# Performance work log

Hardware: AMD Instinct MI355X
Metric: run time of the kernel (lower is better)

The kernel has to match this reference:

```python
import jax, jax.numpy as jnp
import numpy as np

B, S, DIM = 2, 2048, 2048
N_HEADS, N_KV_HEADS = 16, 4
HEAD_DIM = DIM // N_HEADS  # 128
N_REP = N_HEADS // N_KV_HEADS  # 4
ROPE_THETA = 10000.0


def setup_inputs() -> dict:
    key = jax.random.key(0)
    ks = jax.random.split(key, 6)
    x = jax.random.normal(ks[0], (B, S, DIM), dtype=jnp.float32)
    # torch nn.Linear weights are [out_features, in_features]
    sc = 0.02
    wq = jax.random.normal(ks[1], (N_HEADS * HEAD_DIM, DIM), dtype=jnp.float32) * sc
    wk = jax.random.normal(ks[2], (N_KV_HEADS * HEAD_DIM, DIM), dtype=jnp.float32) * sc
    wv = jax.random.normal(ks[3], (N_KV_HEADS * HEAD_DIM, DIM), dtype=jnp.float32) * sc
    wo = jax.random.normal(ks[4], (DIM, N_HEADS * HEAD_DIM), dtype=jnp.float32) * sc
    # precomputed rotary table (freqs_cis in llama): [S, head_dim//2]
    inv_freq = 1.0 / (ROPE_THETA ** (jnp.arange(0, HEAD_DIM, 2, dtype=jnp.float32) / HEAD_DIM))
    t = jnp.arange(S, dtype=jnp.float32)
    freqs = jnp.outer(t, inv_freq)  # [S, head_dim//2]
    freqs_cos = jnp.cos(freqs)
    freqs_sin = jnp.sin(freqs)
    # additive causal mask as passed to SDPA (float, 0 on allowed, -inf-like elsewhere)
    causal = jnp.tril(jnp.ones((S, S), dtype=bool))
    mask = jnp.where(causal, 0.0, -1e9).astype(jnp.float32)
    return {"x": x, "wq": wq, "wk": wk, "wv": wv, "wo": wo,
            "freqs_cos": freqs_cos, "freqs_sin": freqs_sin, "mask": mask}


def _apply_rope(t, cos, sin):
    # t: [B, S, H, D]; cos/sin: [S, D//2] -> complex multiply on adjacent pairs
    tr = t.reshape(*t.shape[:-1], -1, 2)  # [B,S,H,D/2,2]
    tre, tim = tr[..., 0], tr[..., 1]
    c = cos[None, :, None, :]
    s = sin[None, :, None, :]
    out_re = tre * c - tim * s
    out_im = tre * s + tim * c
    return jnp.stack([out_re, out_im], axis=-1).reshape(t.shape)


def reference(x, wq, wk, wv, wo, freqs_cos, freqs_sin, mask):
    Bx, Sx, _ = x.shape
    xq = (x @ wq.T).reshape(Bx, Sx, N_HEADS, HEAD_DIM)
    xk = (x @ wk.T).reshape(Bx, Sx, N_KV_HEADS, HEAD_DIM)
    xv = (x @ wv.T).reshape(Bx, Sx, N_KV_HEADS, HEAD_DIM)
    xq = _apply_rope(xq, freqs_cos, freqs_sin)
    xk = _apply_rope(xk, freqs_cos, freqs_sin)
    # repeat_kv for GQA: [B,S,KV,D] -> [B,S,KV*n_rep,D]
    keys = jnp.repeat(xk, N_REP, axis=2)
    values = jnp.repeat(xv, N_REP, axis=2)
    q = xq.transpose(0, 2, 1, 3)      # [B,H,S,D]
    k = keys.transpose(0, 2, 1, 3)
    v = values.transpose(0, 2, 1, 3)
    scale = 1.0 / jnp.sqrt(jnp.float32(HEAD_DIM))
    scores = jnp.einsum('bhqd,bhkd->bhqk', q, k) * scale + mask[None, None]
    attn = jax.nn.softmax(scores, axis=-1)
    out = jnp.einsum('bhqk,bhkd->bhqd', attn, v)
    out = out.transpose(0, 2, 1, 3).reshape(Bx, Sx, -1)
    return out @ wo.T
```

## Files before the change

kernel.cpp:

```cpp
#include <hip/hip_runtime.h>
#include <hip/hip_bf16.h>

#define B_   2
#define S_   2048
#define DIM_ 2048
#define NH   16
#define NKV  4
#define HD   128
#define QKVN 3072

typedef __attribute__((ext_vector_type(8)))  short  sv8;
typedef __attribute__((ext_vector_type(8)))  ushort usv8;
typedef __attribute__((ext_vector_type(4)))  float  fv4;
typedef __attribute__((ext_vector_type(16))) float  fv16;

__device__ __forceinline__ float fast_exp2(float x) {
  return __builtin_amdgcn_exp2f(x);
}

__device__ __forceinline__ ushort f2bf(float f) {
  __hip_bfloat16 h = __float2bfloat16(f);
  union { __hip_bfloat16 h; ushort u; } c; c.h = h; return c.u;
}
__device__ __forceinline__ float bf2f(ushort u) {
  union { unsigned int i; float f; } c; c.i = ((unsigned)u) << 16; return c.f;
}

__device__ __forceinline__ unsigned int cvtpk(float lo, float hi) {
  unsigned int r;
  asm("v_cvt_pk_bf16_f32 %0, %1, %2" : "=v"(r) : "v"(lo), "v"(hi));
  return r;
}
__device__ __forceinline__ unsigned int xhalf(unsigned int x) {
  return (unsigned int)__shfl_xor((int)x, 32, 64);
}

__device__ __forceinline__ float tmax16(const fv16& v) {
  float a = fmaxf(fmaxf(v[0], v[1]),  fmaxf(v[2], v[3]));
  float b = fmaxf(fmaxf(v[4], v[5]),  fmaxf(v[6], v[7]));
  float c = fmaxf(fmaxf(v[8], v[9]),  fmaxf(v[10], v[11]));
  float d = fmaxf(fmaxf(v[12], v[13]), fmaxf(v[14], v[15]));
  return fmaxf(fmaxf(a, b), fmaxf(c, d));
}
__device__ __forceinline__ float tsum16(const fv16& v) {
  float a = (v[0] + v[1]) + (v[2] + v[3]);
  float b = (v[4] + v[5]) + (v[6] + v[7]);
  float c = (v[8] + v[9]) + (v[10] + v[11]);
  float d = (v[12] + v[13]) + (v[14] + v[15]);
  return (a + b) + (c + d);
}

__device__ __forceinline__ void async16(const void* g, void* l) {
  __builtin_amdgcn_global_load_lds(
      (const __attribute__((address_space(1))) unsigned int*)g,
      (__attribute__((address_space(3))) unsigned int*)l, 16, 0, 0);
}

__global__ void cvt_kernel(const float* __restrict__ in, ushort* __restrict__ out, int n) {
  int i = (blockIdx.x * 256 + threadIdx.x) * 4;
  if (i >= n) return;
  fv4 v = *(const fv4*)(in + i);
  ushort4 o;
  o.x = f2bf(v[0]); o.y = f2bf(v[1]); o.z = f2bf(v[2]); o.w = f2bf(v[3]);
  *(ushort4*)(out + i) = o;
}

__global__ void rope_kernel(const ushort* __restrict__ raw, const float* __restrict__ fc,
                            const float* __restrict__ fs, ushort* __restrict__ out,
                            int heads, int rowstride, float scale) {
  int t = blockIdx.x * 256 + threadIdx.x;
  int grp = t & 15;
  int h   = (t >> 4) % heads;
  int s   = ((t >> 4) / heads) % S_;
  int b   = t / (16 * heads * S_);
  const ushort* src = raw + (size_t)(b * S_ + s) * rowstride + h * HD + grp * 8;
  sv8 v = *(const sv8*)src;
  fv4 c  = *(const fv4*)(fc + s * 64 + grp * 4);
  fv4 sn = *(const fv4*)(fs + s * 64 + grp * 4);
  sv8 o;
#pragma unroll
  for (int p = 0; p < 4; ++p) {
    float re = bf2f((ushort)v[2 * p]);
    float im = bf2f((ushort)v[2 * p + 1]);
    float orr = (re * c[p] - im * sn[p]) * scale;
    float oi  = (re * sn[p] + im * c[p]) * scale;
    o[2 * p]     = (short)f2bf(orr);
    o[2 * p + 1] = (short)f2bf(oi);
  }
  ushort* dst = out + ((size_t)(b * heads + h) * S_ + s) * HD + grp * 8;
  *(sv8*)dst = o;
}

__global__ __launch_bounds__(256) void vtrans_kernel(const ushort* __restrict__ vraw,
                                                     ushort* __restrict__ vt, int rowstride) {
  __shared__ ushort tile[128][136];
  int blk = blockIdx.x;
  int st  = blk & 15;
  int kvb = blk >> 4;
  int kv  = kvb & 3;
  int b   = kvb >> 2;
  int s0  = st << 7;
#pragma unroll
  for (int it = 0; it < 8; ++it) {
    int t = it * 256 + threadIdx.x;
    int srow = t >> 4;
    int d8 = (t & 15) * 8;
    usv8 v = *(const usv8*)(vraw + (size_t)(b * S_ + s0 + srow) * rowstride + kv * HD + d8);
#pragma unroll
    for (int j = 0; j < 8; ++j) tile[d8 + j][srow] = v[j];
  }
  __syncthreads();
#pragma unroll
  for (int it = 0; it < 8; ++it) {
    int t = it * 256 + threadIdx.x;
    int d = t >> 4;
    int s8 = (t & 15) * 8;
    usv8 o;
#pragma unroll
    for (int j = 0; j < 8; ++j) o[j] = tile[d][s8 + j];
    *(usv8*)(vt + ((size_t)(b * NKV + kv) * HD + d) * S_ + s0 + s8) = o;
  }
}

template <typename OutT>
__global__ __launch_bounds__(512, 2) void gemm256(const ushort* __restrict__ A,
                                                  const ushort* __restrict__ Bm,
                                                  OutT* __restrict__ C,
                                                  int M, int N, int K) {
  __shared__ __align__(16) ushort SM[65536];
  int nb = N >> 8;
  int bx = blockIdx.x % nb, by = blockIdx.x / nb;
  int m0 = by << 8, n0 = bx << 8;
  int tid = threadIdx.x;
  int lane = tid & 63, w = tid >> 6;
  int l15 = lane & 15, lg = lane >> 4;
  int wm = (w >> 2) * 128;
  int wn = (w & 3) * 64;
  int pA = (w >> 2);
  int pB = 2 + ((w & 3) >> 1);
  int brow0 = (w & 1) * 64;

  int srow = tid >> 3;
  int cb   = ((tid & 7) * 16) ^ ((srow & 7) << 4);
  const ushort* sA0 = A  + (size_t)(m0 + srow) * K + (cb >> 1);
  const ushort* sB0 = Bm + (size_t)(n0 + srow) * K + (cb >> 1);
  const ushort* srcs[4] = { sA0, sA0 + (size_t)128 * K, sB0, sB0 + (size_t)128 * K };
  size_t rstep = (size_t)64 * K;

  int nkt = K >> 6;

  auto STG = [&](int part, int t, int db) {
    ushort* d0 = SM + db * 32768 + part * 8192 + (w << 9);
    const ushort* s0 = srcs[part] + t * 64;
    async16(s0, d0);
    async16(s0 + rstep, d0 + 4096);
  };

  fv4 acc[8][4] = {};
  sv8 a[4][2], b[2][2], b2[2][2];

#pragma unroll
  for (int p = 0; p < 4; ++p) STG(p, 0, 0);
  {
    int t1 = 1 < nkt ? 1 : 0;
#pragma unroll
    for (int p = 0; p < 4; ++p) STG(p, t1, 1);
  }
  asm volatile("s_waitcnt vmcnt(8)");
  __builtin_amdgcn_s_barrier();

  for (int t = 0; t < nkt; ++t) {
    int db = t & 1;
    int t2 = t + 2 < nkt ? t + 2 : nkt - 1;
    const char* Ab = (const char*)SM + db * 65536 + pA * 16384;
    const char* Bb = (const char*)SM + db * 65536 + pB * 16384;

#pragma unroll
    for (int m = 0; m < 4; ++m)
#pragma unroll
      for (int kk = 0; kk < 2; ++kk) {
        int row = m * 16 + l15;
        a[m][kk] = *(const sv8*)(Ab + row * 128 + ((kk * 64 + lg * 16) ^ ((row & 7) << 4)));
      }
#pragma unroll
    for (int j = 0; j < 2; ++j)
#pragma unroll
      for (int kk = 0; kk < 2; ++kk) {
        int row = brow0 + j * 16 + l15;
        b[j][kk] = *(const sv8*)(Bb + row * 128 + ((kk * 64 + lg * 16) ^ ((row & 7) << 4)));
      }
    __builtin_amdgcn_s_barrier();
    asm volatile("s_waitcnt lgkmcnt(0)");
    __builtin_amdgcn_s_setprio(1);
#pragma unroll
    for (int m = 0; m < 4; ++m)
#pragma unroll
      for (int j = 0; j < 2; ++j)
#pragma unroll
        for (int kk = 0; kk < 2; ++kk)
          acc[m][j] = __builtin_amdgcn_mfma_f32_16x16x32_bf16(a[m][kk], b[j][kk], acc[m][j], 0, 0, 0);
    __builtin_amdgcn_s_setprio(0);
    __builtin_amdgcn_s_barrier();

#pragma unroll
    for (int j = 0; j < 2; ++j)
#pragma unroll
      for (int kk = 0; kk < 2; ++kk) {
        int row = brow0 + (j + 2) * 16 + l15;
        b2[j][kk] = *(const sv8*)(Bb + row * 128 + ((kk * 64 + lg * 16) ^ ((row & 7) << 4)));
      }
    __builtin_amdgcn_s_barrier();
    asm volatile("s_waitcnt lgkmcnt(0)");
    __builtin_amdgcn_s_setprio(1);
#pragma unroll
    for (int m = 0; m < 4; ++m)
#pragma unroll
      for (int j = 0; j < 2; ++j)
#pragma unroll
        for (int kk = 0; kk < 2; ++kk)
          acc[m][j + 2] = __builtin_amdgcn_mfma_f32_16x16x32_bf16(a[m][kk], b2[j][kk], acc[m][j + 2], 0, 0, 0);
    __builtin_amdgcn_s_setprio(0);
    __builtin_amdgcn_s_barrier();

#pragma unroll
    for (int m = 0; m < 4; ++m)
#pragma unroll
      for (int kk = 0; kk < 2; ++kk) {
        int row = 64 + m * 16 + l15;
        a[m][kk] = *(const sv8*)(Ab + row * 128 + ((kk * 64 + lg * 16) ^ ((row & 7) << 4)));
      }
    STG(2, t2, db);
    STG(3, t2, db);
    __builtin_amdgcn_s_barrier();
    asm volatile("s_waitcnt lgkmcnt(0)");
    __builtin_amdgcn_s_setprio(1);
#pragma unroll
    for (int m = 0; m < 4; ++m)
#pragma unroll
      for (int j = 0; j < 2; ++j)
#pragma unroll
        for (int kk = 0; kk < 2; ++kk)
          acc[m + 4][j + 2] = __builtin_amdgcn_mfma_f32_16x16x32_bf16(a[m][kk], b2[j][kk], acc[m + 4][j + 2], 0, 0, 0);
    __builtin_amdgcn_s_setprio(0);
    __builtin_amdgcn_s_barrier();

    STG(0, t2, db);
    STG(1, t2, db);
    asm volatile("s_waitcnt vmcnt(8)");
    __builtin_amdgcn_s_barrier();
    __builtin_amdgcn_s_setprio(1);
#pragma unroll
    for (int m = 0; m < 4; ++m)
#pragma unroll
      for (int j = 0; j < 2; ++j)
#pragma unroll
        for (int kk = 0; kk < 2; ++kk)
          acc[m + 4][j] = __builtin_amdgcn_mfma_f32_16x16x32_bf16(a[m][kk], b[j][kk], acc[m + 4][j], 0, 0, 0);
    __builtin_amdgcn_s_setprio(0);
    __builtin_amdgcn_s_barrier();
  }

  asm volatile("s_waitcnt vmcnt(0)");
#pragma unroll
  for (int m = 0; m < 8; ++m)
#pragma unroll
    for (int j = 0; j < 4; ++j)
#pragma unroll
      for (int r = 0; r < 4; ++r) {
        int row = m0 + wm + m * 16 + lg * 4 + r;
        int col = n0 + wn + j * 16 + l15;
        if constexpr (sizeof(OutT) == 2) C[(size_t)row * N + col] = (OutT)f2bf(acc[m][j][r]);
        else                             C[(size_t)row * N + col] = (OutT)acc[m][j][r];
      }
}

__global__ __launch_bounds__(512, 2) void attn_kernel(const ushort* __restrict__ Q,
                                                      const ushort* __restrict__ Kr,
                                                      const ushort* __restrict__ Vt,
                                                      ushort* __restrict__ O) {
  __shared__ __align__(16) ushort SMEM[65536];

  int blk = blockIdx.x;
  int bh  = blk & 31;
  int pr  = blk >> 5;
  int h   = bh & 15;
  int b   = bh >> 4;
  int kv  = h >> 2;
  int lane = threadIdx.x & 63, w = threadIdx.x >> 6;
  int wg = w & 3, Hf = w >> 2;
  int l31 = lane & 31, hh = lane >> 5;

  const ushort* Qbase = Q  + (size_t)(b * NH  + h ) * S_ * HD;
  const ushort* Kbase = Kr + (size_t)(b * NKV + kv) * S_ * HD;
  const ushort* Vbase = Vt + (size_t)(b * NKV + kv) * HD * S_;

  const ushort* kSrc[4]; ushort* kDst[2][4];
  const ushort* vSrc[4]; ushort* vDst[2][4];
#pragma unroll
  for (int it = 0; it < 4; ++it) {
    int lin = it * 4096 + wg * 1024 + lane * 16;
    { int row = lin >> 8; int cbv = (lin & 255) ^ ((row & 7) << 4);
      kSrc[it] = Kbase + (size_t)row * HD + (cbv >> 1); }
    { int row = lin >> 7; int cbv = (lin & 127) ^ ((row & 7) << 4);
      vSrc[it] = Vbase + (size_t)row * S_ + (cbv >> 1); }
#pragma unroll
    for (int buf = 0; buf < 2; ++buf) {
      kDst[buf][it] = SMEM + Hf * 16384 + buf * 8192 + ((it * 4096 + wg * 1024) >> 1);
      vDst[buf][it] = SMEM + 32768 + Hf * 16384 + buf * 8192 + ((it * 4096 + wg * 1024) >> 1);
    }
  }

  float* cML = (float*)SMEM;
  float* cO  = (float*)SMEM + 512;

  for (int pass = 0; pass < 2; ++pass) {
    int qt = pass ? (15 - pr) : pr;
    int q0 = qt << 7;
    int qrow_w = q0 + wg * 32;
    int myq    = qrow_w + l31;
    int nj     = qt + 1;
    int ktbase = Hf * nj;

    sv8 qf[8];
#pragma unroll
    for (int kk = 0; kk < 8; ++kk)
      qf[kk] = *(const sv8*)(Qbase + (size_t)myq * HD + kk * 16 + hh * 8);

    fv16 oacc[4] = {};
    float mrun = -1e30f, lrun = 0.f;

    {
      size_t k0 = (size_t)ktbase << 6;
#pragma unroll
      for (int it = 0; it < 4; ++it) async16(kSrc[it] + k0 * HD, kDst[0][it]);
#pragma unroll
      for (int it = 0; it < 4; ++it) async16(vSrc[it] + k0,      vDst[0][it]);
    }

    for (int j = 0; j < nj; ++j) {
      int cur = j & 1, nxt = cur ^ 1;
      __syncthreads();
      if (j + 1 < nj) {
        size_t k0n = (size_t)(ktbase + j + 1) << 6;
#pragma unroll
        for (int it = 0; it < 4; ++it) async16(kSrc[it] + k0n * HD, kDst[nxt][it]);
#pragma unroll
        for (int it = 0; it < 4; ++it) async16(vSrc[it] + k0n,      vDst[nxt][it]);
      }
      const char* KsC = (const char*)(SMEM + Hf * 16384 + cur * 8192);
      const char* VsC = (const char*)(SMEM + 32768 + Hf * 16384 + cur * 8192);
      int k0 = (ktbase + j) << 6;

      fv16 sacc[2] = {};
      __builtin_amdgcn_s_setprio(1);
#pragma unroll
      for (int kk = 0; kk < 8; ++kk) {
        int cbq = kk * 32 + hh * 16;
        int r0 = l31, r1 = 32 + l31;
        sv8 kf0 = *(const sv8*)(KsC + r0 * 256 + (cbq ^ ((r0 & 7) << 4)));
        sv8 kf1 = *(const sv8*)(KsC + r1 * 256 + (cbq ^ ((r1 & 7) << 4)));
        sacc[0] = __builtin_amdgcn_mfma_f32_32x32x16_bf16(kf0, qf[kk], sacc[0], 0, 0, 0);
        sacc[1] = __builtin_amdgcn_mfma_f32_32x32x16_bf16(kf1, qf[kk], sacc[1], 0, 0, 0);
      }
      __builtin_amdgcn_s_setprio(0);

      if (k0 + 63 > qrow_w) {
        int thr = myq - k0 - 4 * hh;
#pragma unroll
        for (int t = 0; t < 2; ++t)
#pragma unroll
          for (int r = 0; r < 16; ++r) {
            int kp = t * 32 + (r & 3) + 8 * (r >> 2);
            if (kp > thr) sacc[t][r] = -1e38f;
          }
      }

      float tmax = fmaxf(tmax16(sacc[0]), tmax16(sacc[1]));
      tmax = fmaxf(tmax, __shfl_xor(tmax, 32, 64));

      if (__any(tmax > mrun + 8.0f)) {
        float mnew = fmaxf(mrun, tmax);
        float esc  = fast_exp2(mrun - mnew);
        lrun *= esc;
        float er[16];
#pragma unroll
        for (int r = 0; r < 16; ++r) er[r] = __shfl(esc, (r & 3) + 8 * (r >> 2) + 4 * hh, 64);
#pragma unroll
        for (int d0 = 0; d0 < 4; ++d0)
#pragma unroll
          for (int r = 0; r < 16; ++r) oacc[d0][r] *= er[r];
        mrun = mnew;
      }

#pragma unroll
      for (int t = 0; t < 2; ++t)
#pragma unroll
        for (int r = 0; r < 16; ++r) sacc[t][r] = fast_exp2(sacc[t][r] - mrun);
      float psum = tsum16(sacc[0]) + tsum16(sacc[1]);
      psum += __shfl_xor(psum, 32, 64);
      lrun += psum;

      union Frag { unsigned int u[4]; sv8 v; } pa[4];
#pragma unroll
      for (int t = 0; t < 2; ++t)
#pragma unroll
        for (int half = 0; half < 2; ++half) {
          int cbq = half * 8;
          unsigned int a0 = cvtpk(sacc[t][cbq + 0], sacc[t][cbq + 1]);
          unsigned int a1 = cvtpk(sacc[t][cbq + 2], sacc[t][cbq + 3]);
          unsigned int b0 = cvtpk(sacc[t][cbq + 4], sacc[t][cbq + 5]);
          unsigned int b1 = cvtpk(sacc[t][cbq + 6], sacc[t][cbq + 7]);
          unsigned int a0p = xhalf(a0), a1p = xhalf(a1);
          unsigned int b0p = xhalf(b0), b1p = xhalf(b1);
          pa[2 * t + half].u[0] = hh ? b0p : a0;
          pa[2 * t + half].u[1] = hh ? b1p : a1;
          pa[2 * t + half].u[2] = hh ? b0  : a0p;
          pa[2 * t + half].u[3] = hh ? b1  : a1p;
        }

      __builtin_amdgcn_s_setprio(1);
#pragma unroll
      for (int ks = 0; ks < 4; ++ks) {
        int cbq = ks * 32 + hh * 16;
#pragma unroll
        for (int d0 = 0; d0 < 4; ++d0) {
          int row = d0 * 32 + l31;
          sv8 vf = *(const sv8*)(VsC + row * 128 + (cbq ^ ((row & 7) << 4)));
          oacc[d0] = __builtin_amdgcn_mfma_f32_32x32x16_bf16(pa[ks].v, vf, oacc[d0], 0, 0, 0);
        }
      }
      __builtin_amdgcn_s_setprio(0);
    }

    __syncthreads();
    if (Hf) {
      int base = wg * 64 + lane;
      cML[base * 2]     = mrun;
      cML[base * 2 + 1] = lrun;
      float* dst = cO + base * 65;
#pragma unroll
      for (int d0 = 0; d0 < 4; ++d0)
#pragma unroll
        for (int r = 0; r < 16; ++r) dst[d0 * 16 + r] = oacc[d0][r];
    }
    __syncthreads();
    if (!Hf) {
      int base = wg * 64 + lane;
      float m2 = cML[base * 2], l2 = cML[base * 2 + 1];
      const float* src = cO + base * 65;
      float m  = fmaxf(mrun, m2);
      float e1 = fast_exp2(mrun - m), e2 = fast_exp2(m2 - m);
      float l  = lrun * e1 + l2 * e2;
      float inv = 1.0f / l;
      float f1 = e1 * inv, f2 = e2 * inv;
      float f1b[16], f2b[16];
#pragma unroll
      for (int r = 0; r < 16; ++r) {
        int ro = (r & 3) + 8 * (r >> 2) + 4 * hh;
        f1b[r] = __shfl(f1, ro, 64);
        f2b[r] = __shfl(f2, ro, 64);
      }
#pragma unroll
      for (int r = 0; r < 16; ++r) {
        int q = qrow_w + (r & 3) + 8 * (r >> 2) + 4 * hh;
#pragma unroll
        for (int d0 = 0; d0 < 4; ++d0) {
          int d = d0 * 32 + l31;
          float val = oacc[d0][r] * f1b[r] + src[d0 * 16 + r] * f2b[r];
          O[(size_t)(b * S_ + q) * DIM_ + h * HD + d] = f2bf(val);
        }
      }
    }
    __syncthreads();
  }
}

extern "C" void kernel_launch(void* const* d_in, const int* in_sizes, int n_in,
                              void* d_out, int out_size, void* d_ws, size_t ws_size,
                              hipStream_t stream) {
  const float* x  = (const float*)d_in[0];
  const float* wq = (const float*)d_in[1];
  const float* wk = (const float*)d_in[2];
  const float* wv = (const float*)d_in[3];
  const float* wo = (const float*)d_in[4];
  const float* fc = (const float*)d_in[5];
  const float* fs = (const float*)d_in[6];
  float* out = (float*)d_out;

  char* ws = (char*)d_ws;
  size_t off = 0;
  auto alloc = [&](size_t bytes) -> ushort* {
    ushort* p = (ushort*)(ws + off);
    off += (bytes + 255) & ~(size_t)255;
    return p;
  };
  ushort* xb    = alloc((size_t)B_ * S_ * DIM_ * 2);
  ushort* wqkvb = alloc((size_t)QKVN * DIM_ * 2);
  ushort* wob   = alloc((size_t)DIM_ * DIM_ * 2);
  ushort* qkvr  = alloc((size_t)B_ * S_ * QKVN * 2);
  ushort* qr    = alloc((size_t)B_ * S_ * DIM_ * 2);
  ushort* kr    = alloc((size_t)B_ * S_ * NKV * HD * 2);
  ushort* vtb   = alloc((size_t)B_ * S_ * NKV * HD * 2);
  ushort* obf   = alloc((size_t)B_ * S_ * DIM_ * 2);
  (void)ws_size; (void)n_in; (void)in_sizes; (void)out_size;

  cvt_kernel<<<(B_ * S_ * DIM_) / 1024, 256, 0, stream>>>(x,  xb, B_ * S_ * DIM_);
  cvt_kernel<<<(DIM_ * DIM_) / 1024,     256, 0, stream>>>(wq, wqkvb,                 DIM_ * DIM_);
  cvt_kernel<<<(NKV * HD * DIM_) / 1024, 256, 0, stream>>>(wk, wqkvb + 2048 * DIM_,   NKV * HD * DIM_);
  cvt_kernel<<<(NKV * HD * DIM_) / 1024, 256, 0, stream>>>(wv, wqkvb + 2560 * DIM_,   NKV * HD * DIM_);
  cvt_kernel<<<(DIM_ * DIM_) / 1024,     256, 0, stream>>>(wo, wob, DIM_ * DIM_);

  gemm256<ushort><<<(B_ * S_ / 256) * (QKVN / 256), 512, 0, stream>>>(xb, wqkvb, qkvr,
                                                                     B_ * S_, QKVN, DIM_);

  const float qscale = 0.08838834764831845f * 1.4426950408889634f;
  rope_kernel<<<(B_ * S_ * NH  * 16) / 256, 256, 0, stream>>>(qkvr,        fc, fs, qr, NH,  QKVN, qscale);
  rope_kernel<<<(B_ * S_ * NKV * 16) / 256, 256, 0, stream>>>(qkvr + 2048, fc, fs, kr, NKV, QKVN, 1.0f);
  vtrans_kernel<<<B_ * NKV * (S_ / 128), 256, 0, stream>>>(qkvr + 2560, vtb, QKVN);

  attn_kernel<<<B_ * NH * 8, 512, 0, stream>>>(qr, kr, vtb, obf);

  gemm256<float><<<(B_ * S_ / 256) * (DIM_ / 256), 512, 0, stream>>>(obf, wob, out, B_ * S_, DIM_, DIM_);
}
```

Baseline: 210.5 us.

## Use smaller GEMM tiles so QKV and output projections fill all CUs

New measurement: 196.4 us. 6.7% less time.

```diff
diff --git a/kernel.cpp b/kernel.cpp
--- a/kernel.cpp
+++ b/kernel.cpp
@@ -123,57 +123,128 @@
 }
 
 template <typename OutT>
-__global__ __launch_bounds__(512, 2) void gemm256(const ushort* __restrict__ A,
-                                                  const ushort* __restrict__ Bm,
-                                                  OutT* __restrict__ C,
-                                                  int M, int N, int K) {
-  __shared__ __align__(16) ushort SM[65536];
-  int nb = N >> 8;
+__global__ __launch_bounds__(256) void gemm_bt(const ushort* __restrict__ A,
+                                               const ushort* __restrict__ Bm,
+                                               OutT* __restrict__ C,
+                                               int M, int N, int K) {
+  __shared__ ushort As[128 * 64];
+  __shared__ ushort Bs[128 * 64];
+  int nb = N >> 7;
+  int bx = blockIdx.x % nb;
+  int by = blockIdx.x / nb;
+  int m0 = by << 7, n0 = bx << 7;
+  int lane = threadIdx.x & 63, w = threadIdx.x >> 6;
+  int l15 = lane & 15, lg = lane >> 4;
+  int wm = (w >> 1) * 64, wn = (w & 1) * 64;
+
+  const ushort* aSrc[4]; const ushort* bSrc[4];
+  ushort* aDst[4]; ushort* bDst[4];
+#pragma unroll
+  for (int it = 0; it < 4; ++it) {
+    int lin = it * 4096 + w * 1024 + lane * 16;
+    int row = lin >> 7;
+    int cb  = (lin & 127) ^ ((row & 7) << 4);
+    aSrc[it] = A  + (size_t)(m0 + row) * K + (cb >> 1);
+    bSrc[it] = Bm + (size_t)(n0 + row) * K + (cb >> 1);
+    aDst[it] = As + ((it * 4096 + w * 1024) >> 1);
+    bDst[it] = Bs + ((it * 4096 + w * 1024) >> 1);
+  }
+
+  fv4 acc[4][4] = {};
+
+  for (int kt = 0; kt < K; kt += 64) {
+#pragma unroll
+    for (int it = 0; it < 4; ++it) async16(aSrc[it] + kt, aDst[it]);
+#pragma unroll
+    for (int it = 0; it < 4; ++it) async16(bSrc[it] + kt, bDst[it]);
+    __syncthreads();
+#pragma unroll
+    for (int kk = 0; kk < 2; ++kk) {
+      sv8 af[4], bfr[4];
+#pragma unroll
+      for (int i = 0; i < 4; ++i) {
+        int row = wm + i * 16 + l15;
+        int byt = row * 128 + ((kk * 64 + (lg << 4)) ^ ((row & 7) << 4));
+        af[i] = *(const sv8*)((const char*)As + byt);
+      }
+#pragma unroll
+      for (int j = 0; j < 4; ++j) {
+        int row = wn + j * 16 + l15;
+        int byt = row * 128 + ((kk * 64 + (lg << 4)) ^ ((row & 7) << 4));
+        bfr[j] = *(const sv8*)((const char*)Bs + byt);
+      }
+#pragma unroll
+      for (int i = 0; i < 4; ++i)
+#pragma unroll
+        for (int j = 0; j < 4; ++j)
+          acc[i][j] = __builtin_amdgcn_mfma_f32_16x16x32_bf16(af[i], bfr[j], acc[i][j], 0, 0, 0);
+    }
+    __syncthreads();
+  }
+
+#pragma unroll
+  for (int i = 0; i < 4; ++i)
+#pragma unroll
+    for (int j = 0; j < 4; ++j)
+#pragma unroll
+      for (int r = 0; r < 4; ++r) {
+        int row = m0 + wm + i * 16 + (lg << 2) + r;
+        int col = n0 + wn + j * 16 + l15;
+        if constexpr (sizeof(OutT) == 2) C[(size_t)row * N + col] = (OutT)f2bf(acc[i][j][r]);
+        else                             C[(size_t)row * N + col] = (OutT)acc[i][j][r];
+      }
+}
+
+template <typename OutT>
+__global__ __launch_bounds__(512) void gemmOP(const ushort* __restrict__ A,
+                                              const ushort* __restrict__ Bm,
+                                              OutT* __restrict__ C,
+                                              int M, int N, int K) {
+  __shared__ __align__(16) ushort SM[49152];
+  int nb = N >> 7;
   int bx = blockIdx.x % nb, by = blockIdx.x / nb;
-  int m0 = by << 8, n0 = bx << 8;
+  int m0 = by << 8, n0 = bx << 7;
   int tid = threadIdx.x;
   int lane = tid & 63, w = tid >> 6;
   int l15 = lane & 15, lg = lane >> 4;
   int wm = (w >> 2) * 128;
-  int wn = (w & 3) * 64;
+  int wn = (w & 3) * 32;
   int pA = (w >> 2);
-  int pB = 2 + ((w & 3) >> 1);
-  int brow0 = (w & 1) * 64;
 
   int srow = tid >> 3;
   int cb   = ((tid & 7) * 16) ^ ((srow & 7) << 4);
   const ushort* sA0 = A  + (size_t)(m0 + srow) * K + (cb >> 1);
   const ushort* sB0 = Bm + (size_t)(n0 + srow) * K + (cb >> 1);
-  const ushort* srcs[4] = { sA0, sA0 + (size_t)128 * K, sB0, sB0 + (size_t)128 * K };
+  const ushort* srcs[3] = { sA0, sA0 + (size_t)128 * K, sB0 };
   size_t rstep = (size_t)64 * K;
 
   int nkt = K >> 6;
 
   auto STG = [&](int part, int t, int db) {
-    ushort* d0 = SM + db * 32768 + part * 8192 + (w << 9);
+    ushort* d0 = SM + db * 24576 + part * 8192 + (w << 9);
     const ushort* s0 = srcs[part] + t * 64;
     async16(s0, d0);
     async16(s0 + rstep, d0 + 4096);
   };
 
-  fv4 acc[8][4] = {};
-  sv8 a[4][2], b[2][2], b2[2][2];
-
-#pragma unroll
-  for (int p = 0; p < 4; ++p) STG(p, 0, 0);
+  fv4 acc[8][2] = {};
+  sv8 a[4][2], b[2], b2[2];
+
+#pragma unroll
+  for (int p = 0; p < 3; ++p) STG(p, 0, 0);
   {
     int t1 = 1 < nkt ? 1 : 0;
 #pragma unroll
-    for (int p = 0; p < 4; ++p) STG(p, t1, 1);
-  }
-  asm volatile("s_waitcnt vmcnt(8)");
+    for (int p = 0; p < 3; ++p) STG(p, t1, 1);
+  }
+  asm volatile("s_waitcnt vmcnt(6)");
   __builtin_amdgcn_s_barrier();
 
   for (int t = 0; t < nkt; ++t) {
     int db = t & 1;
     int t2 = t + 2 < nkt ? t + 2 : nkt - 1;
-    const char* Ab = (const char*)SM + db * 65536 + pA * 16384;
-    const char* Bb = (const char*)SM + db * 65536 + pB * 16384;
+    const char* Ab = (const char*)SM + db * 49152 + pA * 16384;
+    const char* Bb = (const char*)SM + db * 49152 + 32768;
 
 #pragma unroll
     for (int m = 0; m < 4; ++m)
@@ -183,42 +254,34 @@
         a[m][kk] = *(const sv8*)(Ab + row * 128 + ((kk * 64 + lg * 16) ^ ((row & 7) << 4)));
       }
 #pragma unroll
-    for (int j = 0; j < 2; ++j)
-#pragma unroll
-      for (int kk = 0; kk < 2; ++kk) {
-        int row = brow0 + j * 16 + l15;
-        b[j][kk] = *(const sv8*)(Bb + row * 128 + ((kk * 64 + lg * 16) ^ ((row & 7) << 4)));
-      }
+    for (int kk = 0; kk < 2; ++kk) {
+      int row = wn + l15;
+      b[kk] = *(const sv8*)(Bb + row * 128 + ((kk * 64 + lg * 16) ^ ((row & 7) << 4)));
+    }
     __builtin_amdgcn_s_barrier();
     asm volatile("s_waitcnt lgkmcnt(0)");
     __builtin_amdgcn_s_setprio(1);
 #pragma unroll
     for (int m = 0; m < 4; ++m)
 #pragma unroll
-      for (int j = 0; j < 2; ++j)
-#pragma unroll
-        for (int kk = 0; kk < 2; ++kk)
-          acc[m][j] = __builtin_amdgcn_mfma_f32_16x16x32_bf16(a[m][kk], b[j][kk], acc[m][j], 0, 0, 0);
+      for (int kk = 0; kk < 2; ++kk)
+        acc[m][0] = __builtin_amdgcn_mfma_f32_16x16x32_bf16(a[m][kk], b[kk], acc[m][0], 0, 0, 0);
     __builtin_amdgcn_s_setprio(0);
     __builtin_amdgcn_s_barrier();
 
 #pragma unroll
-    for (int j = 0; j < 2; ++j)
-#pragma unroll
-      for (int kk = 0; kk < 2; ++kk) {
-        int row = brow0 + (j + 2) * 16 + l15;
-        b2[j][kk] = *(const sv8*)(Bb + row * 128 + ((kk * 64 + lg * 16) ^ ((row & 7) << 4)));
-      }
+    for (int kk = 0; kk < 2; ++kk) {
+      int row = wn + 16 + l15;
+      b2[kk] = *(const sv8*)(Bb + row * 128 + ((kk * 64 + lg * 16) ^ ((row & 7) << 4)));
+    }
     __builtin_amdgcn_s_barrier();
     asm volatile("s_waitcnt lgkmcnt(0)");
     __builtin_amdgcn_s_setprio(1);
 #pragma unroll
     for (int m = 0; m < 4; ++m)
 #pragma unroll
-      for (int j = 0; j < 2; ++j)
-#pragma unroll
-        for (int kk = 0; kk < 2; ++kk)
-          acc[m][j + 2] = __builtin_amdgcn_mfma_f32_16x16x32_bf16(a[m][kk], b2[j][kk], acc[m][j + 2], 0, 0, 0);
+      for (int kk = 0; kk < 2; ++kk)
+        acc[m][1] = __builtin_amdgcn_mfma_f32_16x16x32_bf16(a[m][kk], b2[kk], acc[m][1], 0, 0, 0);
     __builtin_amdgcn_s_setprio(0);
     __builtin_amdgcn_s_barrier();
 
@@ -230,32 +293,27 @@
         a[m][kk] = *(const sv8*)(Ab + row * 128 + ((kk * 64 + lg * 16) ^ ((row & 7) << 4)));
       }
     STG(2, t2, db);
-    STG(3, t2, db);
     __builtin_amdgcn_s_barrier();
     asm volatile("s_waitcnt lgkmcnt(0)");
     __builtin_amdgcn_s_setprio(1);
 #pragma unroll
     for (int m = 0; m < 4; ++m)
 #pragma unroll
-      for (int j = 0; j < 2; ++j)
-#pragma unroll
-        for (int kk = 0; kk < 2; ++kk)
-          acc[m + 4][j + 2] = __builtin_amdgcn_mfma_f32_16x16x32_bf16(a[m][kk], b2[j][kk], acc[m + 4][j + 2], 0, 0, 0);
+      for (int kk = 0; kk < 2; ++kk)
+        acc[m + 4][1] = __builtin_amdgcn_mfma_f32_16x16x32_bf16(a[m][kk], b2[kk], acc[m + 4][1], 0, 0, 0);
     __builtin_amdgcn_s_setprio(0);
     __builtin_amdgcn_s_barrier();
 
     STG(0, t2, db);
     STG(1, t2, db);
-    asm volatile("s_waitcnt vmcnt(8)");
+    asm volatile("s_waitcnt vmcnt(6)");
     __builtin_amdgcn_s_barrier();
     __builtin_amdgcn_s_setprio(1);
 #pragma unroll
     for (int m = 0; m < 4; ++m)
 #pragma unroll
-      for (int j = 0; j < 2; ++j)
-#pragma unroll
-        for (int kk = 0; kk < 2; ++kk)
-          acc[m + 4][j] = __builtin_amdgcn_mfma_f32_16x16x32_bf16(a[m][kk], b[j][kk], acc[m + 4][j], 0, 0, 0);
+      for (int kk = 0; kk < 2; ++kk)
+        acc[m + 4][0] = __builtin_amdgcn_mfma_f32_16x16x32_bf16(a[m][kk], b[kk], acc[m + 4][0], 0, 0, 0);
     __builtin_amdgcn_s_setprio(0);
     __builtin_amdgcn_s_barrier();
   }
@@ -264,7 +322,7 @@
 #pragma unroll
   for (int m = 0; m < 8; ++m)
 #pragma unroll
-    for (int j = 0; j < 4; ++j)
+    for (int j = 0; j < 2; ++j)
 #pragma unroll
       for (int r = 0; r < 4; ++r) {
         int row = m0 + wm + m * 16 + lg * 4 + r;
@@ -510,7 +568,7 @@
   cvt_kernel<<<(NKV * HD * DIM_) / 1024, 256, 0, stream>>>(wv, wqkvb + 2560 * DIM_,   NKV * HD * DIM_);
   cvt_kernel<<<(DIM_ * DIM_) / 1024,     256, 0, stream>>>(wo, wob, DIM_ * DIM_);
 
-  gemm256<ushort><<<(B_ * S_ / 256) * (QKVN / 256), 512, 0, stream>>>(xb, wqkvb, qkvr,
+  gemm_bt<ushort><<<(B_ * S_ / 128) * (QKVN / 128), 256, 0, stream>>>(xb, wqkvb, qkvr,
                                                                      B_ * S_, QKVN, DIM_);
 
   const float qscale = 0.08838834764831845f * 1.4426950408889634f;
@@ -520,5 +578,5 @@
 
   attn_kernel<<<B_ * NH * 8, 512, 0, stream>>>(qr, kr, vtb, obf);
 
-  gemm256<float><<<(B_ * S_ / 256) * (DIM_ / 256), 512, 0, stream>>>(obf, wob, out, B_ * S_, DIM_, DIM_);
-}
+  gemmOP<float><<<(B_ * S_ / 256) * (DIM_ / 128), 512, 0, stream>>>(obf, wob, out, B_ * S_, DIM_, DIM_);
+}
```
